# Kernel optimization log

Hardware: AMD Instinct MI355X
Metric: run time of the kernel (lower is better)

The kernel has to match this reference:

```python
import jax, jax.numpy as jnp
import numpy as np

STRIDES = (8, 16, 32, 64, 128)
SCORE_THR = 0.05
IOU_THR = 0.6
MAX_NUM = 150
USE_CTR = True
B, NC = 64, 20
HW = (128, 64, 32, 16, 8)


def _reshape(feat):
    # [B,C,H,W] -> [B,H*W,C]
    b, c, h, w = feat.shape
    return feat.transpose(0, 2, 3, 1).reshape(b, h * w, c)


def _decode(feat, stride):
    # feat: [B,4,H,W] reg offsets; returns [B,HW,4] boxes (x1,y1,x2,y2)
    _, _, h, w = feat.shape
    xs = jnp.arange(w, dtype=jnp.float32) * stride + (stride // 2)
    ys = jnp.arange(h, dtype=jnp.float32) * stride + (stride // 2)
    yy, xx = jnp.meshgrid(ys, xs, indexing='ij')
    coords = jnp.stack([xx.reshape(-1), yy.reshape(-1)], axis=-1)  # [HW,2]
    off = _reshape(feat) * stride  # [B,HW,4]
    xy1 = coords[None] - off[..., :2]
    xy2 = coords[None] + off[..., 2:]
    return jnp.concatenate([xy1, xy2], axis=-1)


def _nms_single(scores, ids, boxes, valid):
    # scores already sorted descending (from top_k); class-aware offset NMS.
    coord_max = jnp.max(jnp.where(valid[:, None], boxes, -jnp.inf))
    coord_max = jnp.where(jnp.isfinite(coord_max), coord_max, 0.0)
    ob = boxes + (ids.astype(boxes.dtype) * (coord_max + 1.0))[:, None]
    x1, y1, x2, y2 = ob[:, 0], ob[:, 1], ob[:, 2], ob[:, 3]
    areas = (x2 - x1 + 1.0) * (y2 - y1 + 1.0)
    xmin = jnp.maximum(x1[:, None], x1[None, :])
    ymin = jnp.maximum(y1[:, None], y1[None, :])
    xmax = jnp.minimum(x2[:, None], x2[None, :])
    ymax = jnp.minimum(y2[:, None], y2[None, :])
    ow = jnp.clip(xmax - xmin, 0.0)
    oh = jnp.clip(ymax - ymin, 0.0)
    overlap = ow * oh
    union = jnp.clip(areas[:, None] + areas[None, :] - overlap, 1e-10)
    iou = overlap / union  # [N,N]
    n = scores.shape[0]
    idx = jnp.arange(n)

    def body(i, keep):
        sup = keep[i] & (iou[i] > IOU_THR) & (idx > i)
        return keep & ~sup

    return jax.lax.fori_loop(0, n, body, valid)


def setup_inputs() -> dict:
    key = jax.random.key(0)
    ks = jax.random.split(key, 15)
    out = {}
    for li, hw in enumerate(HW):
        out[f'cls{li}'] = jax.random.normal(ks[li], (B, NC, hw, hw), jnp.float32)
        out[f'reg{li}'] = jax.random.uniform(ks[5 + li], (B, 4, hw, hw), jnp.float32)
        out[f'ctr{li}'] = jax.random.normal(ks[10 + li], (B, 1, hw, hw), jnp.float32)
    return out


def reference(cls0, cls1, cls2, cls3, cls4,
              reg0, reg1, reg2, reg3, reg4,
              ctr0, ctr1, ctr2, ctr3, ctr4):
    cls_feats = (cls0, cls1, cls2, cls3, cls4)
    reg_feats = (reg0, reg1, reg2, reg3, reg4)
    ctr_feats = (ctr0, ctr1, ctr2, ctr3, ctr4)

    cls_logits = jnp.concatenate([_reshape(f) for f in cls_feats], axis=1)  # [B,A,NC]
    ctr_logits = jnp.concatenate([_reshape(f) for f in ctr_feats], axis=1)  # [B,A,1]
    cls_preds = jax.nn.sigmoid(cls_logits)
    ctr_preds = jax.nn.sigmoid(ctr_logits)

    cls_scores = jnp.max(cls_preds, axis=-1)  # [B,A]
    cls_ids = jnp.argmax(cls_preds, axis=-1) + 1  # [B,A]
    if USE_CTR:
        cls_scores = jnp.sqrt(cls_scores * ctr_preds[..., 0])

    boxes = jnp.concatenate(
        [_decode(f, s) for f, s in zip(reg_feats, STRIDES)], axis=1)  # [B,A,4]

    top_scores, top_idx = jax.lax.top_k(cls_scores, MAX_NUM)  # sorted desc
    top_ids = jnp.take_along_axis(cls_ids, top_idx, axis=1)
    top_boxes = jnp.take_along_axis(boxes, top_idx[..., None], axis=1)

    valid = top_scores > SCORE_THR
    keep = jax.vmap(_nms_single)(top_scores, top_ids, top_boxes, valid)

    out_scores = jnp.where(keep, top_scores, 0.0)
    out_ids = jnp.where(keep, top_ids, 0)
    out_boxes = jnp.where(keep[..., None], top_boxes, 0.0)
    return out_scores, out_ids, out_boxes, keep
```

## Files before the change

kernel.cpp:

```cpp
#include <hip/hip_runtime.h>
#include <cstdint>
#include <cstddef>

#define NPTS 21824
#define NB   64
#define NCLS 20
#define MAXN 150
#define NCHUNK 11
#define CHSZ 2048
#define CAP  186

typedef unsigned long long u64;
typedef unsigned int u32;


__device__ __forceinline__ u64 bisect_threshold(const u64 (&key)[8], int total,
                                                int (*wcnt)[4], int cap)
{
    const int tid  = threadIdx.x;
    const int lane = tid & 63, wv = tid >> 6;
    u64 T = 0;
    int count = total;
    int it = 0;
    for (int bbit = 62; bbit >= 0; --bbit) {
        if (bbit == 31) bbit = 14;
        if (count <= cap) break;
        u64 Tt = T | (1ull << bbit);
        int c = 0;
        #pragma unroll
        for (int i = 0; i < 8; ++i) c += (key[i] >= Tt) ? 1 : 0;
        for (int off = 32; off; off >>= 1) c += __shfl_xor(c, off);
        if (lane == 0) wcnt[it & 1][wv] = c;
        __syncthreads();
        int tot = wcnt[it & 1][0] + wcnt[it & 1][1]
                + wcnt[it & 1][2] + wcnt[it & 1][3];
        if (tot >= MAXN) { T = Tt; count = tot; }
        ++it;
    }
    return T;
}

__global__ __launch_bounds__(256) void k_part(
    const float* __restrict__ c0, const float* __restrict__ c1,
    const float* __restrict__ c2, const float* __restrict__ c3,
    const float* __restrict__ c4,
    const float* __restrict__ t0, const float* __restrict__ t1,
    const float* __restrict__ t2, const float* __restrict__ t3,
    const float* __restrict__ t4,
    u64* __restrict__ cand)
{
    __shared__ int wcnt[2][4];
    __shared__ int cnt;
    const int tid   = threadIdx.x;
    const int chunk = blockIdx.x;
    const int b     = blockIdx.y;
    const int pl    = tid * 8;
    const int p0    = chunk * CHSZ + pl;

    u64 key[8];
    #pragma unroll
    for (int i = 0; i < 8; ++i) key[i] = 0;

    if (p0 < NPTS) {
        const float* cp; const float* tp; int base; size_t hw;
        if (p0 < 16384)      { cp = c0; tp = t0; base = 0;     hw = 16384; }
        else if (p0 < 20480) { cp = c1; tp = t1; base = 16384; hw = 4096;  }
        else if (p0 < 21504) { cp = c2; tp = t2; base = 20480; hw = 1024;  }
        else if (p0 < 21760) { cp = c3; tp = t3; base = 21504; hw = 256;   }
        else                 { cp = c4; tp = t4; base = 21760; hw = 64;    }
        int q = p0 - base;
        const float* cb = cp + (size_t)b * NCLS * hw + q;

        float4 m0 = *reinterpret_cast<const float4*>(cb);
        float4 m1 = *reinterpret_cast<const float4*>(cb + 4);
        for (int c = 1; c < NCLS; ++c) {
            float4 v0 = *reinterpret_cast<const float4*>(cb + (size_t)c * hw);
            float4 v1 = *reinterpret_cast<const float4*>(cb + (size_t)c * hw + 4);
            m0.x = fmaxf(m0.x, v0.x); m0.y = fmaxf(m0.y, v0.y);
            m0.z = fmaxf(m0.z, v0.z); m0.w = fmaxf(m0.w, v0.w);
            m1.x = fmaxf(m1.x, v1.x); m1.y = fmaxf(m1.y, v1.y);
            m1.z = fmaxf(m1.z, v1.z); m1.w = fmaxf(m1.w, v1.w);
        }
        const float* tb = tp + (size_t)b * hw + q;
        float4 q0 = *reinterpret_cast<const float4*>(tb);
        float4 q1 = *reinterpret_cast<const float4*>(tb + 4);

        float mm[8] = {m0.x, m0.y, m0.z, m0.w, m1.x, m1.y, m1.z, m1.w};
        float cc[8] = {q0.x, q0.y, q0.z, q0.w, q1.x, q1.y, q1.z, q1.w};
        #pragma unroll
        for (int i = 0; i < 8; ++i) {
            float best = 1.0f / (1.0f + expf(-mm[i]));
            float sct  = 1.0f / (1.0f + expf(-cc[i]));
            float sc   = sqrtf(__fmul_rn(best, sct));
            key[i] = ((u64)__float_as_uint(sc) << 32)
                   | (u32)(21823 - (p0 + i));
        }
    }

    u64 T = bisect_threshold(key, CHSZ, wcnt, CAP);

    if (tid == 0) cnt = 0;
    __syncthreads();
    u64* outp = cand + ((size_t)b * NCHUNK + chunk) * CAP;
    #pragma unroll
    for (int i = 0; i < 8; ++i) {
        if (key[i] >= T) {
            int pos = atomicAdd(&cnt, 1);
            if (pos < CAP) outp[pos] = key[i];
        }
    }
    __syncthreads();
    for (int i = cnt + tid; i < CAP; i += 256) outp[i] = 0;
}

__global__ __launch_bounds__(256) void k_final(
    const float* __restrict__ c0, const float* __restrict__ c1,
    const float* __restrict__ c2, const float* __restrict__ c3,
    const float* __restrict__ c4,
    const float* __restrict__ r0, const float* __restrict__ r1,
    const float* __restrict__ r2, const float* __restrict__ r3,
    const float* __restrict__ r4,
    const u64* __restrict__ cand,
    float* __restrict__ out)
{
    const int NC2 = NCHUNK * CAP;
    __shared__ int wcnt[2][4];
    __shared__ int cnt;
    __shared__ u64 win[CAP];
    __shared__ u64 srt[MAXN];
    __shared__ float bx0[MAXN], bx1[MAXN], bx2[MAXN], bx3[MAXN];
    __shared__ float ox1[MAXN], oy1[MAXN], ox2[MAXN], oy2[MAXN], area[MAXN];
    __shared__ float sc[MAXN];
    __shared__ int   idv[MAXN];
    __shared__ u64 sup[MAXN][3];
    __shared__ u64 keepw[3];
    __shared__ float shcmax;
    __shared__ float wmax[4];

    const int b = blockIdx.x, tid = threadIdx.x;

    u64 key[8];
    #pragma unroll
    for (int j = 0; j < 8; ++j) {
        int i = j * 256 + tid;
        key[j] = (i < NC2) ? cand[(size_t)b * NC2 + i] : 0ull;
    }

    u64 T = bisect_threshold(key, CHSZ, wcnt, CAP);

    if (tid == 0) cnt = 0;
    if (tid < MAXN) srt[tid] = 0ull;
    __syncthreads();
    #pragma unroll
    for (int j = 0; j < 8; ++j) {
        if (key[j] >= T) {
            int pos = atomicAdd(&cnt, 1);
            if (pos < CAP) win[pos] = key[j];
        }
    }
    __syncthreads();
    int C = min(cnt, CAP);
    if (tid < C) {
        u64 mk = win[tid]; int r = 0;
        for (int j = 0; j < C; ++j) r += (win[j] > mk) ? 1 : 0;
        if (r < MAXN) srt[r] = mk;
    }
    __syncthreads();

    if (tid < MAXN) {
        u64 kk = srt[tid];
        sc[tid] = __uint_as_float((u32)(kk >> 32));
        int p   = 21823 - (int)(kk & 0x7FFFu);

        const float* rp; const float* cp; int base, dim, lg, st;
        if (p < 16384)      { rp = r0; cp = c0; base = 0;     dim = 128; lg = 7; st = 8;   }
        else if (p < 20480) { rp = r1; cp = c1; base = 16384; dim = 64;  lg = 6; st = 16;  }
        else if (p < 21504) { rp = r2; cp = c2; base = 20480; dim = 32;  lg = 5; st = 32;  }
        else if (p < 21760) { rp = r3; cp = c3; base = 21504; dim = 16;  lg = 4; st = 64;  }
        else                { rp = r4; cp = c4; base = 21760; dim = 8;   lg = 3; st = 128; }

        int q = p - base;
        size_t hw = (size_t)dim * dim;

        const float* cb = cp + (size_t)b * NCLS * hw + q;
        float best = -1.0f; int bi = 0;
        for (int c = 0; c < NCLS; ++c) {
            float v  = cb[(size_t)c * hw];
            float sg = 1.0f / (1.0f + expf(-v));
            if (sg > best) { best = sg; bi = c; }
        }
        idv[tid] = bi + 1;

        int y = q >> lg;
        int x = q & (dim - 1);
        float s  = (float)st;
        float cx = (float)(x * st + (st >> 1));
        float cy = (float)(y * st + (st >> 1));
        const float* rg = rp + (size_t)b * 4 * hw + q;
        float a0 = rg[0], a1 = rg[hw], a2 = rg[2 * hw], a3 = rg[3 * hw];
        bx0[tid] = __fsub_rn(cx, __fmul_rn(a0, s));
        bx1[tid] = __fsub_rn(cy, __fmul_rn(a1, s));
        bx2[tid] = __fadd_rn(cx, __fmul_rn(a2, s));
        bx3[tid] = __fadd_rn(cy, __fmul_rn(a3, s));
    }
    __syncthreads();

    float m = -INFINITY;
    if (tid < MAXN && sc[tid] > 0.05f)
        m = fmaxf(fmaxf(bx0[tid], bx1[tid]), fmaxf(bx2[tid], bx3[tid]));
    #pragma unroll
    for (int off = 32; off >= 1; off >>= 1) m = fmaxf(m, __shfl_xor(m, off));
    if ((tid & 63) == 0) wmax[tid >> 6] = m;
    if (tid < 192) {
        bool val = (tid < MAXN) && (sc[tid] > 0.05f);
        u64 mask = __ballot(val);
        if ((tid & 63) == 0) keepw[tid >> 6] = mask;
    }
    __syncthreads();
    if (tid == 0) {
        float mm = fmaxf(fmaxf(wmax[0], wmax[1]), fmaxf(wmax[2], wmax[3]));
        shcmax = isfinite(mm) ? mm : 0.0f;
    }
    __syncthreads();

    float cm1 = __fadd_rn(shcmax, 1.0f);
    if (tid < MAXN) {
        float off = __fmul_rn((float)idv[tid], cm1);
        float X1 = __fadd_rn(bx0[tid], off);
        float Y1 = __fadd_rn(bx1[tid], off);
        float X2 = __fadd_rn(bx2[tid], off);
        float Y2 = __fadd_rn(bx3[tid], off);
        ox1[tid] = X1; oy1[tid] = Y1; ox2[tid] = X2; oy2[tid] = Y2;
        area[tid] = __fmul_rn(__fadd_rn(__fsub_rn(X2, X1), 1.0f),
                              __fadd_rn(__fsub_rn(Y2, Y1), 1.0f));
    }
    __syncthreads();

    for (int t = tid; t < MAXN * 3; t += 256) {
        int i = t / 3;
        int w = t - i * 3;
        float x1i = ox1[i], y1i = oy1[i], x2i = ox2[i], y2i = oy2[i], ai = area[i];
        u64 bits = 0ull;
        for (int e = 0; e < 64; ++e) {
            int j = w * 64 + e;
            if (j >= MAXN) break;
            float xmin = fmaxf(x1i, ox1[j]);
            float ymin = fmaxf(y1i, oy1[j]);
            float xmax = fminf(x2i, ox2[j]);
            float ymax = fminf(y2i, oy2[j]);
            float ow = fmaxf(__fsub_rn(xmax, xmin), 0.0f);
            float oh = fmaxf(__fsub_rn(ymax, ymin), 0.0f);
            float ov = __fmul_rn(ow, oh);
            float un = fmaxf(__fsub_rn(__fadd_rn(ai, area[j]), ov), 1e-10f);
            float iou = __fdiv_rn(ov, un);
            if (iou > 0.6f) bits |= (1ull << e);
        }
        sup[i][w] = bits;
    }
    __syncthreads();

    if (tid < 64) {
        const int l = tid;
        u64 kw   = (l < 3) ? keepw[l]  : 0ull;
        u64 scur = (l < 3) ? sup[0][l] : 0ull;
        for (int i = 0; i < MAXN; ++i) {
            u64 snext = (l < 3 && i + 1 < MAXN) ? sup[i + 1][l] : 0ull;
            u64 kwwi = __shfl(kw, i >> 6);
            if ((kwwi >> (i & 63)) & 1ull) {
                int lo = l * 64;
                u64 allow;
                if (i < lo)            allow = ~0ull;
                else if (i - lo >= 63) allow = 0ull;
                else                   allow = ~((1ull << (i - lo + 1)) - 1ull);
                kw &= ~(scur & allow);
            }
            scur = snext;
        }
        if (l < 3) keepw[l] = kw;
    }
    __syncthreads();

    if (tid < MAXN) {
        bool kp = (keepw[tid >> 6] >> (tid & 63)) & 1ull;
        int o = b * MAXN + tid;
        float* oSc = out;
        float* oId = out + NB * MAXN;
        float* oBx = out + 2 * NB * MAXN;
        float* oKp = out + 2 * NB * MAXN + NB * MAXN * 4;
        oSc[o] = kp ? sc[tid] : 0.0f;
        oId[o] = kp ? (float)idv[tid] : 0.0f;
        oBx[o * 4 + 0] = kp ? bx0[tid] : 0.0f;
        oBx[o * 4 + 1] = kp ? bx1[tid] : 0.0f;
        oBx[o * 4 + 2] = kp ? bx2[tid] : 0.0f;
        oBx[o * 4 + 3] = kp ? bx3[tid] : 0.0f;
        oKp[o] = kp ? 1.0f : 0.0f;
    }
}

extern "C" void kernel_launch(void* const* d_in, const int* in_sizes, int n_in,
                              void* d_out, int out_size, void* d_ws, size_t ws_size,
                              hipStream_t stream)
{
    const float* cls[5]; const float* reg[5]; const float* ctr[5];
    for (int li = 0; li < 5; ++li) {
        cls[li] = (const float*)d_in[3 * li + 0];
        reg[li] = (const float*)d_in[3 * li + 1];
        ctr[li] = (const float*)d_in[3 * li + 2];
    }

    u64* cand = (u64*)d_ws;

    dim3 g1(NCHUNK, NB);
    k_part<<<g1, 256, 0, stream>>>(cls[0], cls[1], cls[2], cls[3], cls[4],
                                   ctr[0], ctr[1], ctr[2], ctr[3], ctr[4],
                                   cand);
    k_final<<<NB, 256, 0, stream>>>(cls[0], cls[1], cls[2], cls[3], cls[4],
                                    reg[0], reg[1], reg[2], reg[3], reg[4],
                                    cand, (float*)d_out);
}
```

Baseline: 254.2 us.

## Fuse partition and final kernels via last-block counter; use radix select

Merges the per-chunk candidate partition and the per-batch final selection/NMS into a single kernel. The last block to finish for each batch, detected with an atomic counter, does the final stage, so the second launch and its gap go away. The bit-by-bit bisection threshold search is replaced by an 8-bit radix select built from shared-memory histograms, which needs fewer barrier rounds. In exchange it adds a tiny zeroing kernel, thread fences, and final-stage work that runs on only one block per batch.

After: 342.3 us. +34.6%, slower.

```diff
diff --git a/kernel.cpp b/kernel.cpp
--- a/kernel.cpp
+++ b/kernel.cpp
@@ -14,118 +14,85 @@
 typedef unsigned int u32;
 
 
-__device__ __forceinline__ u64 bisect_threshold(const u64 (&key)[8], int total,
-                                                int (*wcnt)[4], int cap)
+__device__ __forceinline__ u64 radix_select(const u64 (&key)[8],
+                                            u32 (*hist)[256], int* sres)
 {
-    const int tid  = threadIdx.x;
-    const int lane = tid & 63, wv = tid >> 6;
-    u64 T = 0;
-    int count = total;
-    int it = 0;
-    for (int bbit = 62; bbit >= 0; --bbit) {
-        if (bbit == 31) bbit = 14;
-        if (count <= cap) break;
-        u64 Tt = T | (1ull << bbit);
-        int c = 0;
+    const int tid = threadIdx.x;
+    const int wv  = tid >> 6;
+    u64 P = 0, T = 0;
+    int r = MAXN, above = 0;
+    for (int pass = 0; pass < 8; ++pass) {
+        const int sh = 56 - 8 * pass;
+        hist[0][tid] = 0; hist[1][tid] = 0; hist[2][tid] = 0; hist[3][tid] = 0;
+        __syncthreads();
         #pragma unroll
-        for (int i = 0; i < 8; ++i) c += (key[i] >= Tt) ? 1 : 0;
-        for (int off = 32; off; off >>= 1) c += __shfl_xor(c, off);
-        if (lane == 0) wcnt[it & 1][wv] = c;
-        __syncthreads();
-        int tot = wcnt[it & 1][0] + wcnt[it & 1][1]
-                + wcnt[it & 1][2] + wcnt[it & 1][3];
-        if (tot >= MAXN) { T = Tt; count = tot; }
-        ++it;
+        for (int i = 0; i < 8; ++i) {
+            u64 k = key[i];
+            if (pass == 0 || (k >> (sh + 8)) == P)
+                atomicAdd(&hist[wv][(u32)(k >> sh) & 255u], 1u);
+        }
+        __syncthreads();
+        if (tid < 64) {
+            int h0 = hist[0][4*tid+0] + hist[1][4*tid+0] + hist[2][4*tid+0] + hist[3][4*tid+0];
+            int h1 = hist[0][4*tid+1] + hist[1][4*tid+1] + hist[2][4*tid+1] + hist[3][4*tid+1];
+            int h2 = hist[0][4*tid+2] + hist[1][4*tid+2] + hist[2][4*tid+2] + hist[3][4*tid+2];
+            int h3 = hist[0][4*tid+3] + hist[1][4*tid+3] + hist[2][4*tid+3] + hist[3][4*tid+3];
+            int s  = h0 + h1 + h2 + h3;
+            int S  = s;
+            #pragma unroll
+            for (int off = 1; off < 64; off <<= 1) {
+                int v = __shfl_down(S, off);
+                if (tid + off < 64) S += v;
+            }
+            u64 mask = __ballot(S >= r);
+            int L = 63 - __builtin_clzll(mask);
+            if (tid == L) {
+                int cum = S - s;
+                int hh[4] = {h0, h1, h2, h3};
+                int sel = 4*L, selcnt = 0, rn = r, an = cum;
+                #pragma unroll
+                for (int j = 3; j >= 0; --j) {
+                    if (cum + hh[j] >= r) {
+                        sel = 4*L + j; selcnt = hh[j]; rn = r - cum; an = cum;
+                        break;
+                    }
+                    cum += hh[j];
+                }
+                sres[0] = sel; sres[1] = rn; sres[2] = an; sres[3] = selcnt;
+            }
+        }
+        __syncthreads();
+        P = (P << 8) | (u64)(u32)sres[0];
+        r = sres[1];
+        above += sres[2];
+        int count = above + sres[3];
+        if (count <= CAP) { T = P << sh; break; }
     }
     return T;
 }
 
-__global__ __launch_bounds__(256) void k_part(
-    const float* __restrict__ c0, const float* __restrict__ c1,
-    const float* __restrict__ c2, const float* __restrict__ c3,
-    const float* __restrict__ c4,
-    const float* __restrict__ t0, const float* __restrict__ t1,
-    const float* __restrict__ t2, const float* __restrict__ t3,
-    const float* __restrict__ t4,
-    u64* __restrict__ cand)
+__global__ void k_zero(u32* __restrict__ c)
 {
-    __shared__ int wcnt[2][4];
-    __shared__ int cnt;
-    const int tid   = threadIdx.x;
-    const int chunk = blockIdx.x;
-    const int b     = blockIdx.y;
-    const int pl    = tid * 8;
-    const int p0    = chunk * CHSZ + pl;
-
-    u64 key[8];
-    #pragma unroll
-    for (int i = 0; i < 8; ++i) key[i] = 0;
-
-    if (p0 < NPTS) {
-        const float* cp; const float* tp; int base; size_t hw;
-        if (p0 < 16384)      { cp = c0; tp = t0; base = 0;     hw = 16384; }
-        else if (p0 < 20480) { cp = c1; tp = t1; base = 16384; hw = 4096;  }
-        else if (p0 < 21504) { cp = c2; tp = t2; base = 20480; hw = 1024;  }
-        else if (p0 < 21760) { cp = c3; tp = t3; base = 21504; hw = 256;   }
-        else                 { cp = c4; tp = t4; base = 21760; hw = 64;    }
-        int q = p0 - base;
-        const float* cb = cp + (size_t)b * NCLS * hw + q;
-
-        float4 m0 = *reinterpret_cast<const float4*>(cb);
-        float4 m1 = *reinterpret_cast<const float4*>(cb + 4);
-        for (int c = 1; c < NCLS; ++c) {
-            float4 v0 = *reinterpret_cast<const float4*>(cb + (size_t)c * hw);
-            float4 v1 = *reinterpret_cast<const float4*>(cb + (size_t)c * hw + 4);
-            m0.x = fmaxf(m0.x, v0.x); m0.y = fmaxf(m0.y, v0.y);
-            m0.z = fmaxf(m0.z, v0.z); m0.w = fmaxf(m0.w, v0.w);
-            m1.x = fmaxf(m1.x, v1.x); m1.y = fmaxf(m1.y, v1.y);
-            m1.z = fmaxf(m1.z, v1.z); m1.w = fmaxf(m1.w, v1.w);
-        }
-        const float* tb = tp + (size_t)b * hw + q;
-        float4 q0 = *reinterpret_cast<const float4*>(tb);
-        float4 q1 = *reinterpret_cast<const float4*>(tb + 4);
-
-        float mm[8] = {m0.x, m0.y, m0.z, m0.w, m1.x, m1.y, m1.z, m1.w};
-        float cc[8] = {q0.x, q0.y, q0.z, q0.w, q1.x, q1.y, q1.z, q1.w};
-        #pragma unroll
-        for (int i = 0; i < 8; ++i) {
-            float best = 1.0f / (1.0f + expf(-mm[i]));
-            float sct  = 1.0f / (1.0f + expf(-cc[i]));
-            float sc   = sqrtf(__fmul_rn(best, sct));
-            key[i] = ((u64)__float_as_uint(sc) << 32)
-                   | (u32)(21823 - (p0 + i));
-        }
-    }
-
-    u64 T = bisect_threshold(key, CHSZ, wcnt, CAP);
-
-    if (tid == 0) cnt = 0;
-    __syncthreads();
-    u64* outp = cand + ((size_t)b * NCHUNK + chunk) * CAP;
-    #pragma unroll
-    for (int i = 0; i < 8; ++i) {
-        if (key[i] >= T) {
-            int pos = atomicAdd(&cnt, 1);
-            if (pos < CAP) outp[pos] = key[i];
-        }
-    }
-    __syncthreads();
-    for (int i = cnt + tid; i < CAP; i += 256) outp[i] = 0;
+    c[threadIdx.x] = 0u;
 }
 
-__global__ __launch_bounds__(256) void k_final(
+__global__ __launch_bounds__(256) void k_fused(
     const float* __restrict__ c0, const float* __restrict__ c1,
     const float* __restrict__ c2, const float* __restrict__ c3,
     const float* __restrict__ c4,
     const float* __restrict__ r0, const float* __restrict__ r1,
     const float* __restrict__ r2, const float* __restrict__ r3,
     const float* __restrict__ r4,
-    const u64* __restrict__ cand,
+    const float* __restrict__ t0, const float* __restrict__ t1,
+    const float* __restrict__ t2, const float* __restrict__ t3,
+    const float* __restrict__ t4,
+    u64* __restrict__ cand, u32* __restrict__ done,
     float* __restrict__ out)
 {
-    const int NC2 = NCHUNK * CAP;
-    __shared__ int wcnt[2][4];
+    __shared__ u32 hist[4][256];
+    __shared__ int sres[4];
     __shared__ int cnt;
+    __shared__ int lastflag;
     __shared__ u64 win[CAP];
     __shared__ u64 srt[MAXN];
     __shared__ float bx0[MAXN], bx1[MAXN], bx2[MAXN], bx3[MAXN];
@@ -137,8 +104,80 @@
     __shared__ float shcmax;
     __shared__ float wmax[4];
 
-    const int b = blockIdx.x, tid = threadIdx.x;
-
+    const int tid   = threadIdx.x;
+    const int chunk = blockIdx.x;
+    const int b     = blockIdx.y;
+
+    {
+        const int pl = tid * 8;
+        const int p0 = chunk * CHSZ + pl;
+        u64 key[8];
+        #pragma unroll
+        for (int i = 0; i < 8; ++i) key[i] = 0;
+
+        if (p0 < NPTS) {
+            const float* cp; const float* tp; int base; size_t hw;
+            if (p0 < 16384)      { cp = c0; tp = t0; base = 0;     hw = 16384; }
+            else if (p0 < 20480) { cp = c1; tp = t1; base = 16384; hw = 4096;  }
+            else if (p0 < 21504) { cp = c2; tp = t2; base = 20480; hw = 1024;  }
+            else if (p0 < 21760) { cp = c3; tp = t3; base = 21504; hw = 256;   }
+            else                 { cp = c4; tp = t4; base = 21760; hw = 64;    }
+            int q = p0 - base;
+            const float* cb = cp + (size_t)b * NCLS * hw + q;
+
+            float4 m0 = *reinterpret_cast<const float4*>(cb);
+            float4 m1 = *reinterpret_cast<const float4*>(cb + 4);
+            for (int c = 1; c < NCLS; ++c) {
+                float4 v0 = *reinterpret_cast<const float4*>(cb + (size_t)c * hw);
+                float4 v1 = *reinterpret_cast<const float4*>(cb + (size_t)c * hw + 4);
+                m0.x = fmaxf(m0.x, v0.x); m0.y = fmaxf(m0.y, v0.y);
+                m0.z = fmaxf(m0.z, v0.z); m0.w = fmaxf(m0.w, v0.w);
+                m1.x = fmaxf(m1.x, v1.x); m1.y = fmaxf(m1.y, v1.y);
+                m1.z = fmaxf(m1.z, v1.z); m1.w = fmaxf(m1.w, v1.w);
+            }
+            const float* tb = tp + (size_t)b * hw + q;
+            float4 q0 = *reinterpret_cast<const float4*>(tb);
+            float4 q1 = *reinterpret_cast<const float4*>(tb + 4);
+
+            float mm[8] = {m0.x, m0.y, m0.z, m0.w, m1.x, m1.y, m1.z, m1.w};
+            float cc[8] = {q0.x, q0.y, q0.z, q0.w, q1.x, q1.y, q1.z, q1.w};
+            #pragma unroll
+            for (int i = 0; i < 8; ++i) {
+                float best = 1.0f / (1.0f + expf(-mm[i]));
+                float sct  = 1.0f / (1.0f + expf(-cc[i]));
+                float s    = sqrtf(__fmul_rn(best, sct));
+                key[i] = ((u64)__float_as_uint(s) << 32)
+                       | (u32)(21823 - (p0 + i));
+            }
+        }
+
+        u64 T = radix_select(key, hist, sres);
+
+        if (tid == 0) cnt = 0;
+        __syncthreads();
+        u64* outp = cand + ((size_t)b * NCHUNK + chunk) * CAP;
+        #pragma unroll
+        for (int i = 0; i < 8; ++i) {
+            if (key[i] >= T) {
+                int pos = atomicAdd(&cnt, 1);
+                if (pos < CAP) outp[pos] = key[i];
+            }
+        }
+        __syncthreads();
+        for (int i = cnt + tid; i < CAP; i += 256) outp[i] = 0;
+    }
+
+    __threadfence();
+    __syncthreads();
+    if (tid == 0) {
+        u32 old = atomicAdd(&done[b], 1u);
+        lastflag = (old == NCHUNK - 1);
+    }
+    __syncthreads();
+    if (!lastflag) return;
+    __threadfence();
+
+    const int NC2 = NCHUNK * CAP;
     u64 key[8];
     #pragma unroll
     for (int j = 0; j < 8; ++j) {
@@ -146,7 +185,7 @@
         key[j] = (i < NC2) ? cand[(size_t)b * NC2 + i] : 0ull;
     }
 
-    u64 T = bisect_threshold(key, CHSZ, wcnt, CAP);
+    u64 T = radix_select(key, hist, sres);
 
     if (tid == 0) cnt = 0;
     if (tid < MAXN) srt[tid] = 0ull;
@@ -308,13 +347,15 @@
         ctr[li] = (const float*)d_in[3 * li + 2];
     }
 
+    const size_t CAND_BYTES = (size_t)NB * NCHUNK * CAP * sizeof(u64);
     u64* cand = (u64*)d_ws;
-
-    dim3 g1(NCHUNK, NB);
-    k_part<<<g1, 256, 0, stream>>>(cls[0], cls[1], cls[2], cls[3], cls[4],
+    u32* done = (u32*)((char*)d_ws + CAND_BYTES);
+
+    k_zero<<<1, NB, 0, stream>>>(done);
+
+    dim3 g(NCHUNK, NB);
+    k_fused<<<g, 256, 0, stream>>>(cls[0], cls[1], cls[2], cls[3], cls[4],
+                                   reg[0], reg[1], reg[2], reg[3], reg[4],
                                    ctr[0], ctr[1], ctr[2], ctr[3], ctr[4],
-                                   cand);
-    k_final<<<NB, 256, 0, stream>>>(cls[0], cls[1], cls[2], cls[3], cls[4],
-                                    reg[0], reg[1], reg[2], reg[3], reg[4],
-                                    cand, (float*)d_out);
+                                   cand, done, (float*)d_out);
 }
```

## Split final kernel into selection and wide 1024-thread output kernel

Applied to the files above, without the earlier changes.

The per-image final kernel becomes two kernels. k_sel does the threshold bisection and rank sort and writes the sorted top-150 keys to workspace. k_out runs with 1024 threads: four threads share each candidate's 20-class argmax through packed score/index keys, separate threads decode boxes in parallel, and the IoU bitmask pass needs only one iteration per thread. This shortens the latency-bound serial gathers, at the cost of one extra launch and a global round trip for the sorted keys.

After: 246.7 us. 3.0% less time.

```diff
diff --git a/kernel.cpp b/kernel.cpp
--- a/kernel.cpp
+++ b/kernel.cpp
@@ -113,21 +113,55 @@
     for (int i = cnt + tid; i < CAP; i += 256) outp[i] = 0;
 }
 
-__global__ __launch_bounds__(256) void k_final(
+__global__ __launch_bounds__(256) void k_sel(
+    const u64* __restrict__ cand, u64* __restrict__ srt_g)
+{
+    const int NC2 = NCHUNK * CAP;
+    __shared__ int wcnt[2][4];
+    __shared__ int cnt;
+    __shared__ u64 win[CAP];
+
+    const int b = blockIdx.x, tid = threadIdx.x;
+
+    u64 key[8];
+    #pragma unroll
+    for (int j = 0; j < 8; ++j) {
+        int i = j * 256 + tid;
+        key[j] = (i < NC2) ? cand[(size_t)b * NC2 + i] : 0ull;
+    }
+
+    u64 T = bisect_threshold(key, CHSZ, wcnt, CAP);
+
+    if (tid == 0) cnt = 0;
+    __syncthreads();
+    #pragma unroll
+    for (int j = 0; j < 8; ++j) {
+        if (key[j] >= T) {
+            int pos = atomicAdd(&cnt, 1);
+            if (pos < CAP) win[pos] = key[j];
+        }
+    }
+    __syncthreads();
+    int C = min(cnt, CAP);
+    if (tid < C) {
+        u64 mk = win[tid]; int r = 0;
+        for (int j = 0; j < C; ++j) r += (win[j] > mk) ? 1 : 0;
+        if (r < MAXN) srt_g[(size_t)b * MAXN + r] = mk;
+    }
+}
+
+__global__ __launch_bounds__(1024) void k_out(
     const float* __restrict__ c0, const float* __restrict__ c1,
     const float* __restrict__ c2, const float* __restrict__ c3,
     const float* __restrict__ c4,
     const float* __restrict__ r0, const float* __restrict__ r1,
     const float* __restrict__ r2, const float* __restrict__ r3,
     const float* __restrict__ r4,
-    const u64* __restrict__ cand,
+    const u64* __restrict__ srt_g,
     float* __restrict__ out)
 {
-    const int NC2 = NCHUNK * CAP;
-    __shared__ int wcnt[2][4];
-    __shared__ int cnt;
-    __shared__ u64 win[CAP];
-    __shared__ u64 srt[MAXN];
+    __shared__ int   parr[MAXN];
+    __shared__ u64   pid[MAXN][4];
     __shared__ float bx0[MAXN], bx1[MAXN], bx2[MAXN], bx3[MAXN];
     __shared__ float ox1[MAXN], oy1[MAXN], ox2[MAXN], oy2[MAXN], area[MAXN];
     __shared__ float sc[MAXN];
@@ -135,73 +169,69 @@
     __shared__ u64 sup[MAXN][3];
     __shared__ u64 keepw[3];
     __shared__ float shcmax;
-    __shared__ float wmax[4];
+    __shared__ float wmax[16];
 
     const int b = blockIdx.x, tid = threadIdx.x;
 
-    u64 key[8];
-    #pragma unroll
-    for (int j = 0; j < 8; ++j) {
-        int i = j * 256 + tid;
-        key[j] = (i < NC2) ? cand[(size_t)b * NC2 + i] : 0ull;
-    }
-
-    u64 T = bisect_threshold(key, CHSZ, wcnt, CAP);
-
-    if (tid == 0) cnt = 0;
-    if (tid < MAXN) srt[tid] = 0ull;
-    __syncthreads();
-    #pragma unroll
-    for (int j = 0; j < 8; ++j) {
-        if (key[j] >= T) {
-            int pos = atomicAdd(&cnt, 1);
-            if (pos < CAP) win[pos] = key[j];
-        }
-    }
-    __syncthreads();
-    int C = min(cnt, CAP);
-    if (tid < C) {
-        u64 mk = win[tid]; int r = 0;
-        for (int j = 0; j < C; ++j) r += (win[j] > mk) ? 1 : 0;
-        if (r < MAXN) srt[r] = mk;
-    }
-    __syncthreads();
-
     if (tid < MAXN) {
-        u64 kk = srt[tid];
-        sc[tid] = __uint_as_float((u32)(kk >> 32));
-        int p   = 21823 - (int)(kk & 0x7FFFu);
-
-        const float* rp; const float* cp; int base, dim, lg, st;
-        if (p < 16384)      { rp = r0; cp = c0; base = 0;     dim = 128; lg = 7; st = 8;   }
-        else if (p < 20480) { rp = r1; cp = c1; base = 16384; dim = 64;  lg = 6; st = 16;  }
-        else if (p < 21504) { rp = r2; cp = c2; base = 20480; dim = 32;  lg = 5; st = 32;  }
-        else if (p < 21760) { rp = r3; cp = c3; base = 21504; dim = 16;  lg = 4; st = 64;  }
-        else                { rp = r4; cp = c4; base = 21760; dim = 8;   lg = 3; st = 128; }
-
-        int q = p - base;
-        size_t hw = (size_t)dim * dim;
-
-        const float* cb = cp + (size_t)b * NCLS * hw + q;
+        u64 kk = srt_g[(size_t)b * MAXN + tid];
+        sc[tid]   = __uint_as_float((u32)(kk >> 32));
+        parr[tid] = 21823 - (int)(kk & 0x7FFFu);
+    }
+    __syncthreads();
+
+    if (tid < MAXN * 4) {
+        int w = tid >> 2, g = tid & 3;
+        int p = parr[w];
+        const float* cp; int base; size_t hw;
+        if (p < 16384)      { cp = c0; base = 0;     hw = 16384; }
+        else if (p < 20480) { cp = c1; base = 16384; hw = 4096;  }
+        else if (p < 21504) { cp = c2; base = 20480; hw = 1024;  }
+        else if (p < 21760) { cp = c3; base = 21504; hw = 256;   }
+        else                { cp = c4; base = 21760; hw = 64;    }
+        const float* cb = cp + (size_t)b * NCLS * hw + (p - base);
         float best = -1.0f; int bi = 0;
-        for (int c = 0; c < NCLS; ++c) {
+        #pragma unroll
+        for (int j = 0; j < 5; ++j) {
+            int c = g * 5 + j;
             float v  = cb[(size_t)c * hw];
             float sg = 1.0f / (1.0f + expf(-v));
             if (sg > best) { best = sg; bi = c; }
         }
-        idv[tid] = bi + 1;
-
+        pid[w][g] = ((u64)__float_as_uint(best) << 32) | (u32)(31 - bi);
+    } else if (tid < MAXN * 4 + MAXN) {
+        int w = tid - MAXN * 4;
+        int p = parr[w];
+        const float* rp; int base, dim, lg, st;
+        if (p < 16384)      { rp = r0; base = 0;     dim = 128; lg = 7; st = 8;   }
+        else if (p < 20480) { rp = r1; base = 16384; dim = 64;  lg = 6; st = 16;  }
+        else if (p < 21504) { rp = r2; base = 20480; dim = 32;  lg = 5; st = 32;  }
+        else if (p < 21760) { rp = r3; base = 21504; dim = 16;  lg = 4; st = 64;  }
+        else                { rp = r4; base = 21760; dim = 8;   lg = 3; st = 128; }
+        int q = p - base;
         int y = q >> lg;
         int x = q & (dim - 1);
         float s  = (float)st;
         float cx = (float)(x * st + (st >> 1));
         float cy = (float)(y * st + (st >> 1));
+        size_t hw = (size_t)dim * dim;
         const float* rg = rp + (size_t)b * 4 * hw + q;
         float a0 = rg[0], a1 = rg[hw], a2 = rg[2 * hw], a3 = rg[3 * hw];
-        bx0[tid] = __fsub_rn(cx, __fmul_rn(a0, s));
-        bx1[tid] = __fsub_rn(cy, __fmul_rn(a1, s));
-        bx2[tid] = __fadd_rn(cx, __fmul_rn(a2, s));
-        bx3[tid] = __fadd_rn(cy, __fmul_rn(a3, s));
+        bx0[w] = __fsub_rn(cx, __fmul_rn(a0, s));
+        bx1[w] = __fsub_rn(cy, __fmul_rn(a1, s));
+        bx2[w] = __fadd_rn(cx, __fmul_rn(a2, s));
+        bx3[w] = __fadd_rn(cy, __fmul_rn(a3, s));
+    }
+    __syncthreads();
+
+    if (tid < MAXN) {
+        u64 m0 = pid[tid][0], m1 = pid[tid][1];
+        u64 m2 = pid[tid][2], m3 = pid[tid][3];
+        u64 mbest = m0;
+        if (m1 > mbest) mbest = m1;
+        if (m2 > mbest) mbest = m2;
+        if (m3 > mbest) mbest = m3;
+        idv[tid] = (31 - (int)(mbest & 31u)) + 1;
     }
     __syncthreads();
 
@@ -218,7 +248,9 @@
     }
     __syncthreads();
     if (tid == 0) {
-        float mm = fmaxf(fmaxf(wmax[0], wmax[1]), fmaxf(wmax[2], wmax[3]));
+        float mm = -INFINITY;
+        #pragma unroll
+        for (int w = 0; w < 16; ++w) mm = fmaxf(mm, wmax[w]);
         shcmax = isfinite(mm) ? mm : 0.0f;
     }
     __syncthreads();
@@ -236,9 +268,9 @@
     }
     __syncthreads();
 
-    for (int t = tid; t < MAXN * 3; t += 256) {
-        int i = t / 3;
-        int w = t - i * 3;
+    if (tid < MAXN * 3) {
+        int i = tid / 3;
+        int w = tid - i * 3;
         float x1i = ox1[i], y1i = oy1[i], x2i = ox2[i], y2i = oy2[i], ai = area[i];
         u64 bits = 0ull;
         for (int e = 0; e < 64; ++e) {
@@ -308,13 +340,16 @@
         ctr[li] = (const float*)d_in[3 * li + 2];
     }
 
-    u64* cand = (u64*)d_ws;
+    const size_t CAND_BYTES = (size_t)NB * NCHUNK * CAP * sizeof(u64);
+    u64* cand  = (u64*)d_ws;
+    u64* srt_g = (u64*)((char*)d_ws + CAND_BYTES);
 
     dim3 g1(NCHUNK, NB);
     k_part<<<g1, 256, 0, stream>>>(cls[0], cls[1], cls[2], cls[3], cls[4],
                                    ctr[0], ctr[1], ctr[2], ctr[3], ctr[4],
                                    cand);
-    k_final<<<NB, 256, 0, stream>>>(cls[0], cls[1], cls[2], cls[3], cls[4],
-                                    reg[0], reg[1], reg[2], reg[3], reg[4],
-                                    cand, (float*)d_out);
-}
+    k_sel<<<NB, 256, 0, stream>>>(cand, srt_g);
+    k_out<<<NB, 1024, 0, stream>>>(cls[0], cls[1], cls[2], cls[3], cls[4],
+                                   reg[0], reg[1], reg[2], reg[3], reg[4],
+                                   srt_g, (float*)d_out);
+}
```
